# Performance work log

Hardware: AMD Instinct MI355X
Metric: run time of the kernel (lower is better)

Reference implementation:

```python
import jax, jax.numpy as jnp
import numpy as np

EMBED_DIM = 1024
NUM_HEADS = 16
HEAD_DIM = EMBED_DIM // NUM_HEADS
SCALE = HEAD_DIM ** -0.5


def setup_inputs() -> dict:
    key = jax.random.key(0)
    k_x, k_qkv, k_w, k_b = jax.random.split(key, 4)
    B, N = 2, 2048
    x = jax.random.normal(k_x, (B, N, EMBED_DIM), dtype=jnp.float32)
    # nn.Linear weights stored as (out, in); init with small normal
    w_qkv = jax.random.normal(k_qkv, (3 * EMBED_DIM, EMBED_DIM), dtype=jnp.float32) * (EMBED_DIM ** -0.5)
    w_out = jax.random.normal(k_w, (EMBED_DIM, EMBED_DIM), dtype=jnp.float32) * (EMBED_DIM ** -0.5)
    b_out = jax.random.normal(k_b, (EMBED_DIM,), dtype=jnp.float32) * 0.02
    return {"x": x, "w_qkv": w_qkv, "w_out": w_out, "b_out": b_out}


def reference(x, w_qkv, w_out, b_out):
    B, N, _ = x.shape
    # qkv: (B, N, 3*E) -> (B, N, 3, H, Dh)
    qkv = jnp.einsum('bne,fe->bnf', x, w_qkv).reshape(B, N, 3, NUM_HEADS, HEAD_DIM)
    q, k, v = qkv[:, :, 0], qkv[:, :, 1], qkv[:, :, 2]
    scores = jnp.einsum('bnhd,bmhd->bhnm', q, k) * SCALE
    attn = jax.nn.softmax(scores, axis=-1)  # dropout is identity in eval mode
    out = jnp.einsum('bhnm,bmhd->bnhd', attn, v).reshape(B, N, EMBED_DIM)
    return jnp.einsum('bne,fe->bnf', out, w_out) + b_out
```

## Files before the change

### kernel.cpp

```cpp
#include <hip/hip_runtime.h>
#include <stdint.h>
#include <stddef.h>

#define SEQ   2048
#define BATCH 2
#define NTOK  (SEQ*BATCH)
#define EMB   1024
#define QKVN  3072
#define NH    16
#define HD    64

typedef __bf16 bf16x8 __attribute__((ext_vector_type(8)));
typedef float  f32x4  __attribute__((ext_vector_type(4)));

__device__ __forceinline__ unsigned short f2b(float f) {
  union { float f; uint32_t u; } v; v.f = f;
  uint32_t r = v.u + 0x7fffu + ((v.u >> 16) & 1u);
  return (unsigned short)(r >> 16);
}

#define GLOAD_LDS16(gp, lp)                                                    \
  __builtin_amdgcn_global_load_lds(                                            \
      (__attribute__((address_space(1))) void*)(gp),                           \
      (__attribute__((address_space(3))) void*)(lp), 16, 0, 0)

__global__ void cvt_bf16_kernel(const float* __restrict__ in,
                                unsigned short* __restrict__ out, int n4) {
  int i = blockIdx.x * blockDim.x + threadIdx.x;
  if (i < n4) {
    float4 v = ((const float4*)in)[i];
    ushort4 o;
    o.x = f2b(v.x); o.y = f2b(v.y); o.z = f2b(v.z); o.w = f2b(v.w);
    ((ushort4*)out)[i] = o;
  }
}

__global__ __launch_bounds__(256) void gemm_bt(
    const unsigned short* __restrict__ A,
    const unsigned short* __restrict__ B,
    unsigned short* __restrict__ Cb,
    float* __restrict__ Cf,
    const float* __restrict__ bias,
    unsigned short* __restrict__ vt,
    int M, int N, int K, int mode)
{
  __shared__ unsigned short As[128*32];
  __shared__ unsigned short Bs[128*32];

  const int tid  = threadIdx.x;
  const int wave = tid >> 6, lane = tid & 63;
  const int l16  = lane & 15, quad = lane >> 4;
  const int tm = blockIdx.x * 128, tn = blockIdx.y * 128;
  const int wm = (wave & 1) * 64,  wn = (wave >> 1) * 64;

  f32x4 acc[4][4] = {};

  for (int k0 = 0; k0 < K; k0 += 32) {
    __syncthreads();
#pragma unroll
    for (int j = 0; j < 2; ++j) {
      const int e   = (wave*2 + j)*512 + lane*8;
      const int row = e >> 5, kk = e & 31;
      GLOAD_LDS16(A + (size_t)(tm + row)*K + (k0 + kk), As + (wave*2 + j)*512);
      GLOAD_LDS16(B + (size_t)(tn + row)*K + (k0 + kk), Bs + (wave*2 + j)*512);
    }
    __syncthreads();

    bf16x8 af[4], bf[4];
#pragma unroll
    for (int i = 0; i < 4; ++i) {
      af[i] = *(const bf16x8*)(As + (wm + i*16 + l16)*32 + quad*8);
      bf[i] = *(const bf16x8*)(Bs + (wn + i*16 + l16)*32 + quad*8);
    }
#pragma unroll
    for (int mi = 0; mi < 4; ++mi)
#pragma unroll
      for (int ni = 0; ni < 4; ++ni)
        acc[mi][ni] = __builtin_amdgcn_mfma_f32_16x16x32_bf16(af[mi], bf[ni], acc[mi][ni], 0, 0, 0);
  }

  if (mode == 1) {
#pragma unroll
    for (int mi = 0; mi < 4; ++mi)
#pragma unroll
      for (int ni = 0; ni < 4; ++ni)
#pragma unroll
        for (int r = 0; r < 4; ++r) {
          const int row = tm + wm + mi*16 + quad*4 + r;
          const int col = tn + wn + ni*16 + l16;
          Cf[(size_t)row*N + col] = acc[mi][ni][r] + bias[col];
        }
  } else {
    if (tn < 2048) {
#pragma unroll
      for (int mi = 0; mi < 4; ++mi)
#pragma unroll
        for (int ni = 0; ni < 4; ++ni)
#pragma unroll
          for (int r = 0; r < 4; ++r) {
            const int row = tm + wm + mi*16 + quad*4 + r;
            const int col = tn + wn + ni*16 + l16;
            Cb[(size_t)row*2048 + col] = f2b(acc[mi][ni][r]);
          }
    } else {
#pragma unroll
      for (int mi = 0; mi < 4; ++mi)
#pragma unroll
        for (int ni = 0; ni < 4; ++ni) {
          const int f    = tn + wn + ni*16 + l16 - 2048;
          const int row0 = tm + wm + mi*16 + quad*4;
          const int bb   = row0 >> 11;
          const int n0   = row0 & 2047;
          ushort4 pv;
          pv.x = f2b(acc[mi][ni][0]); pv.y = f2b(acc[mi][ni][1]);
          pv.z = f2b(acc[mi][ni][2]); pv.w = f2b(acc[mi][ni][3]);
          *(ushort4*)(vt + ((size_t)(bb*1024 + f))*2048 + n0) = pv;
        }
    }
  }
}

__global__ __launch_bounds__(256) void attn_kernel(
    const unsigned short* __restrict__ qk,
    const unsigned short* __restrict__ vT,
    unsigned short* __restrict__ aout)
{
  __shared__ unsigned short Ks[2][64*64];
  __shared__ unsigned short Vt[2][64*64];
  __shared__ unsigned short Pl[4*16*64];

  const int tid  = threadIdx.x;
  const int wave = tid >> 6, lane = tid & 63;
  const int l16  = lane & 15, quad = lane >> 4;

  const int flat = blockIdx.x;
  const int xcd  = flat & 7;
  const int idx  = flat >> 3;
  const int bh   = xcd*4 + (idx >> 5);
  const int qt   = idx & 31;
  const int b  = bh >> 4, h = bh & 15;
  const size_t tok0 = (size_t)b * SEQ;
  const int qrow0 = qt*64 + wave*16;
  const int swz = (l16 & 7) << 3;

  const int sp0  = wave*64 + lane;
  const int sp1  = 256 + wave*64 + lane;
  const int srow0 = sp0 >> 3, sc0 = ((sp0 & 7) ^ (srow0 & 7)) << 3;
  const int srow1 = sp1 >> 3, sc1 = ((sp1 & 7) ^ (srow1 & 7)) << 3;
  const unsigned short* kbase = qk + tok0*2048 + 1024 + h*64;
  const unsigned short* vbase = vT + ((size_t)(b*1024 + h*64))*2048;
  const int ldst0 = (wave*64)*8;
  const int ldst1 = (256 + wave*64)*8;

#define STAGE(dst, kk0s)                                                      \
  do {                                                                        \
    GLOAD_LDS16(kbase + (size_t)((kk0s) + srow0)*2048 + sc0, Ks[dst] + ldst0);\
    GLOAD_LDS16(vbase + (size_t)srow0*2048 + (kk0s) + sc0,   Vt[dst] + ldst0);\
    GLOAD_LDS16(kbase + (size_t)((kk0s) + srow1)*2048 + sc1, Ks[dst] + ldst1);\
    GLOAD_LDS16(vbase + (size_t)srow1*2048 + (kk0s) + sc1,   Vt[dst] + ldst1);\
  } while (0)

  bf16x8 qf[2];
  {
    const unsigned short* qp = qk + (tok0 + qrow0 + l16)*2048 + h*64;
#pragma unroll
    for (int ks = 0; ks < 2; ++ks) {
      bf16x8 t = *(const bf16x8*)(qp + ks*32 + quad*8);
#pragma unroll
      for (int j = 0; j < 8; ++j) t[j] = (__bf16)((float)t[j] * 0.125f);
      qf[ks] = t;
    }
  }

  f32x4 oacc[4] = {};
  float l_run = 0.f;
  unsigned short* Pw = Pl + wave*(16*64);
  const float LOG2E = 1.44269504f;
  const float OFF2  = 17.3123405f;

  STAGE(0, 0);
  __syncthreads();

  for (int kb = 0; kb < SEQ/64; ++kb) {
    const int cur = kb & 1;
    if (kb + 1 < SEQ/64) STAGE(cur ^ 1, (kb + 1)*64);

    const unsigned short* Kc = Ks[cur];
    const unsigned short* Vc = Vt[cur];

    f32x4 s[4] = {};
    __builtin_amdgcn_s_setprio(1);
#pragma unroll
    for (int ks = 0; ks < 2; ++ks)
#pragma unroll
      for (int mf = 0; mf < 4; ++mf) {
        bf16x8 kf = *(const bf16x8*)(Kc + (mf*16 + l16)*64 + (((ks*4 + quad) ^ (l16 & 7)) << 3));
        s[mf] = __builtin_amdgcn_mfma_f32_16x16x32_bf16(kf, qf[ks], s[mf], 0, 0, 0);
      }
    __builtin_amdgcn_s_setprio(0);

    {
      float rs = l_run;
#pragma unroll
      for (int mf = 0; mf < 4; ++mf) {
        union { float f; uint32_t u; } a0, a1, a2, a3;
        a0.f = __builtin_amdgcn_exp2f(fmaf(s[mf][0], LOG2E, -OFF2));
        a1.f = __builtin_amdgcn_exp2f(fmaf(s[mf][1], LOG2E, -OFF2));
        a2.f = __builtin_amdgcn_exp2f(fmaf(s[mf][2], LOG2E, -OFF2));
        a3.f = __builtin_amdgcn_exp2f(fmaf(s[mf][3], LOG2E, -OFF2));
        rs += (a0.f + a1.f) + (a2.f + a3.f);
        uint2 pk;
        pk.x = __builtin_amdgcn_perm(a1.u, a0.u, 0x07060302u);
        pk.y = __builtin_amdgcn_perm(a3.u, a2.u, 0x07060302u);
        *(uint2*)(Pw + l16*64 + ((mf*16 + quad*4) ^ swz)) = pk;
      }
      l_run = rs;
    }

    __builtin_amdgcn_s_setprio(1);
#pragma unroll
    for (int ks = 0; ks < 2; ++ks) {
      bf16x8 pf = *(const bf16x8*)(Pw + l16*64 + ((ks*32 + quad*8) ^ swz));
#pragma unroll
      for (int mf = 0; mf < 4; ++mf) {
        bf16x8 vf = *(const bf16x8*)(Vc + (mf*16 + l16)*64 + (((ks*4 + quad) ^ (l16 & 7)) << 3));
        oacc[mf] = __builtin_amdgcn_mfma_f32_16x16x32_bf16(vf, pf, oacc[mf], 0, 0, 0);
      }
    }
    __builtin_amdgcn_s_setprio(0);

    __syncthreads();
  }
#undef STAGE

  {
    float l = l_run;
    l += __shfl_xor(l, 16);
    l += __shfl_xor(l, 32);
    const float inv = 1.0f / l;
    const size_t trow = tok0 + qrow0 + l16;
#pragma unroll
    for (int mf = 0; mf < 4; ++mf) {
      ushort4 ov;
      ov.x = f2b(oacc[mf][0] * inv);
      ov.y = f2b(oacc[mf][1] * inv);
      ov.z = f2b(oacc[mf][2] * inv);
      ov.w = f2b(oacc[mf][3] * inv);
      *(ushort4*)(aout + trow*EMB + h*64 + mf*16 + quad*4) = ov;
    }
  }
}

extern "C" void kernel_launch(void* const* d_in, const int* in_sizes, int n_in,
                              void* d_out, int out_size, void* d_ws, size_t ws_size,
                              hipStream_t stream) {
  const float* x     = (const float*)d_in[0];
  const float* w_qkv = (const float*)d_in[1];
  const float* w_out = (const float*)d_in[2];
  const float* b_out = (const float*)d_in[3];

  char* ws = (char*)d_ws;
  unsigned short* xb    = (unsigned short*)(ws);
  unsigned short* wqkvb = (unsigned short*)(ws + 8388608);
  unsigned short* woutb = (unsigned short*)(ws + 14680064);
  unsigned short* qkb   = (unsigned short*)(ws + 16777216);
  unsigned short* vTb   = (unsigned short*)(ws + 33554432);
  unsigned short* aob   = (unsigned short*)(ws + 41943040);

  cvt_bf16_kernel<<<(NTOK*EMB/4 + 255)/256, 256, 0, stream>>>(x, xb, NTOK*EMB/4);
  cvt_bf16_kernel<<<(QKVN*EMB/4 + 255)/256, 256, 0, stream>>>(w_qkv, wqkvb, QKVN*EMB/4);
  cvt_bf16_kernel<<<(EMB*EMB/4 + 255)/256, 256, 0, stream>>>(w_out, woutb, EMB*EMB/4);

  gemm_bt<<<dim3(NTOK/128, QKVN/128), 256, 0, stream>>>(
      xb, wqkvb, qkb, nullptr, nullptr, vTb, NTOK, QKVN, EMB, 2);

  attn_kernel<<<dim3(1024), 256, 0, stream>>>(qkb, vTb, aob);

  gemm_bt<<<dim3(NTOK/128, EMB/128), 256, 0, stream>>>(
      aob, woutb, nullptr, (float*)d_out, b_out, nullptr, NTOK, EMB, EMB, 1);
}
```

Before: 207.2 us.

## Double GEMM K-tile with XOR-swizzled LDS and merge conversion kernels

The three fp32-to-bf16 conversion launches become one kernel that picks its source and destination by global index. The GEMM now stages a 64-wide K slice per iteration instead of 32, halving the number of barrier pairs, and uses an XOR swizzle on 16-byte chunks to avoid LDS bank conflicts on the wider rows. LDS use per block doubles, which may lower occupancy, and the swizzle must match between the global-to-LDS writes and the fragment reads.

```diff
diff --git a/kernel.cpp b/kernel.cpp
--- a/kernel.cpp
+++ b/kernel.cpp
@@ -24,15 +24,21 @@
       (__attribute__((address_space(1))) void*)(gp),                           \
       (__attribute__((address_space(3))) void*)(lp), 16, 0, 0)
 
-__global__ void cvt_bf16_kernel(const float* __restrict__ in,
-                                unsigned short* __restrict__ out, int n4) {
+__global__ void cvt3_kernel(const float* __restrict__ x,
+                            const float* __restrict__ wq,
+                            const float* __restrict__ wo,
+                            unsigned short* __restrict__ xb,
+                            unsigned short* __restrict__ wqb,
+                            unsigned short* __restrict__ wob) {
   int i = blockIdx.x * blockDim.x + threadIdx.x;
-  if (i < n4) {
-    float4 v = ((const float4*)in)[i];
-    ushort4 o;
-    o.x = f2b(v.x); o.y = f2b(v.y); o.z = f2b(v.z); o.w = f2b(v.w);
-    ((ushort4*)out)[i] = o;
-  }
+  const float* in; unsigned short* out; int k;
+  if (i < 1048576)              { in = x;  out = xb;  k = i; }
+  else if (i < 1048576+786432)  { in = wq; out = wqb; k = i - 1048576; }
+  else                          { in = wo; out = wob; k = i - (1048576+786432); }
+  float4 v = ((const float4*)in)[k];
+  ushort4 o;
+  o.x = f2b(v.x); o.y = f2b(v.y); o.z = f2b(v.z); o.w = f2b(v.w);
+  ((ushort4*)out)[k] = o;
 }
 
 __global__ __launch_bounds__(256) void gemm_bt(
@@ -44,8 +50,8 @@
     unsigned short* __restrict__ vt,
     int M, int N, int K, int mode)
 {
-  __shared__ unsigned short As[128*32];
-  __shared__ unsigned short Bs[128*32];
+  __shared__ unsigned short As[128*64];
+  __shared__ unsigned short Bs[128*64];
 
   const int tid  = threadIdx.x;
   const int wave = tid >> 6, lane = tid & 63;
@@ -55,28 +61,33 @@
 
   f32x4 acc[4][4] = {};
 
-  for (int k0 = 0; k0 < K; k0 += 32) {
+  for (int k0 = 0; k0 < K; k0 += 64) {
     __syncthreads();
 #pragma unroll
-    for (int j = 0; j < 2; ++j) {
-      const int e   = (wave*2 + j)*512 + lane*8;
-      const int row = e >> 5, kk = e & 31;
-      GLOAD_LDS16(A + (size_t)(tm + row)*K + (k0 + kk), As + (wave*2 + j)*512);
-      GLOAD_LDS16(B + (size_t)(tn + row)*K + (k0 + kk), Bs + (wave*2 + j)*512);
+    for (int j = 0; j < 4; ++j) {
+      const int p   = (wave*4 + j)*64 + lane;
+      const int row = p >> 3;
+      const int c   = ((p & 7) ^ (row & 7)) << 3;
+      GLOAD_LDS16(A + (size_t)(tm + row)*K + (k0 + c), As + (wave*4 + j)*512);
+      GLOAD_LDS16(B + (size_t)(tn + row)*K + (k0 + c), Bs + (wave*4 + j)*512);
     }
     __syncthreads();
 
-    bf16x8 af[4], bf[4];
-#pragma unroll
-    for (int i = 0; i < 4; ++i) {
-      af[i] = *(const bf16x8*)(As + (wm + i*16 + l16)*32 + quad*8);
-      bf[i] = *(const bf16x8*)(Bs + (wn + i*16 + l16)*32 + quad*8);
-    }
-#pragma unroll
-    for (int mi = 0; mi < 4; ++mi)
-#pragma unroll
-      for (int ni = 0; ni < 4; ++ni)
-        acc[mi][ni] = __builtin_amdgcn_mfma_f32_16x16x32_bf16(af[mi], bf[ni], acc[mi][ni], 0, 0, 0);
+#pragma unroll
+    for (int ks = 0; ks < 2; ++ks) {
+      bf16x8 af[4], bf[4];
+#pragma unroll
+      for (int i = 0; i < 4; ++i) {
+        const int ca = ((ks*4 + quad) ^ (l16 & 7)) << 3;
+        af[i] = *(const bf16x8*)(As + (wm + i*16 + l16)*64 + ca);
+        bf[i] = *(const bf16x8*)(Bs + (wn + i*16 + l16)*64 + ca);
+      }
+#pragma unroll
+      for (int mi = 0; mi < 4; ++mi)
+#pragma unroll
+        for (int ni = 0; ni < 4; ++ni)
+          acc[mi][ni] = __builtin_amdgcn_mfma_f32_16x16x32_bf16(af[mi], bf[ni], acc[mi][ni], 0, 0, 0);
+    }
   }
 
   if (mode == 1) {
@@ -267,9 +278,7 @@
   unsigned short* vTb   = (unsigned short*)(ws + 33554432);
   unsigned short* aob   = (unsigned short*)(ws + 41943040);
 
-  cvt_bf16_kernel<<<(NTOK*EMB/4 + 255)/256, 256, 0, stream>>>(x, xb, NTOK*EMB/4);
-  cvt_bf16_kernel<<<(QKVN*EMB/4 + 255)/256, 256, 0, stream>>>(w_qkv, wqkvb, QKVN*EMB/4);
-  cvt_bf16_kernel<<<(EMB*EMB/4 + 255)/256, 256, 0, stream>>>(w_out, woutb, EMB*EMB/4);
+  cvt3_kernel<<<8192, 256, 0, stream>>>(x, w_qkv, w_out, xb, wqkvb, woutb);
 
   gemm_bt<<<dim3(NTOK/128, QKVN/128), 256, 0, stream>>>(
       xb, wqkvb, qkb, nullptr, nullptr, vTb, NTOK, QKVN, EMB, 2);
```

Result: no change. 205.1 us (-1.0%).
